# Optimization experiments

Hardware: AMD Instinct MI355X
Metric: run time of the kernel (lower is better)

## Reference

```python
import jax, jax.numpy as jnp
import numpy as np

EPS = 0.001  # epsilon used by both custom layer norms in the source
B, T, D, H, O = 64, 1024, 128, 256, 64


def setup_inputs() -> dict:
    key = jax.random.key(0)
    ks = jax.random.split(key, 8)
    s = 0.05
    return {
        "x": jax.random.normal(ks[0], (B, T, D), jnp.float32),
        "Wi": jax.random.normal(ks[1], (4 * H, D), jnp.float32) * s,   # input_weights
        "bi": jax.random.normal(ks[2], (4 * H,), jnp.float32) * s,
        "Wh": jax.random.normal(ks[3], (4 * H, H), jnp.float32) * s,   # hidden_weights
        "bh": jax.random.normal(ks[4], (4 * H,), jnp.float32) * s,
        "lna_gamma": jnp.ones((4 * H,), jnp.float32),
        "lna_beta": jnp.zeros((4 * H,), jnp.float32),
        "ln_gamma": jnp.ones((H,), jnp.float32),
        "ln_beta": jnp.zeros((H,), jnp.float32),
        "Wf": jax.random.normal(ks[5], (O, H), jnp.float32) * s,       # fc
        "bf": jax.random.normal(ks[6], (O,), jnp.float32) * s,
    }


def _ln(x, gamma, beta):
    # custom layer norm: mean/var over last axis, eps=1e-3 (no Bessel correction)
    m = jnp.mean(x, axis=-1, keepdims=True)
    xs = x - m
    v = jnp.mean(xs * xs, axis=-1, keepdims=True)
    return gamma * (xs / jnp.sqrt(v + EPS)) + beta


def reference(x, Wi, bi, Wh, bh, lna_gamma, lna_beta, ln_gamma, ln_beta, Wf, bf):
    b, t, d = x.shape
    h = Wh.shape[1]
    # precompute input projections for all timesteps: (T, B, 4H)
    xproj = jnp.einsum('btd,gd->tbg', x, Wi) + bi

    def step(carry, xp_t):
        hx, cx = carry                              # (B, H) each
        gates = xp_t + hx @ Wh.T + bh               # (B, 4H)
        # layer_norm_all: normalize each of the 4 gate blocks over H
        g4 = gates.reshape(b, 4, h)
        m = jnp.mean(g4, axis=-1, keepdims=True)
        gs = g4 - m
        v = jnp.mean(gs * gs, axis=-1, keepdims=True)
        gates = (gs / jnp.sqrt(v + EPS)).reshape(b, 4 * h) * lna_gamma + lna_beta
        ig, fg, cg, og = jnp.split(gates, 4, axis=1)
        ig = jax.nn.sigmoid(ig)
        fg = jax.nn.sigmoid(fg)
        cg = jnp.tanh(cg)
        og = jax.nn.sigmoid(og)
        cy = fg * cx + ig * cg
        hy = og * jnp.tanh(_ln(cy, ln_gamma, ln_beta))
        return (hy, cy), hy

    h0 = jnp.zeros((b, h), x.dtype)
    c0 = jnp.zeros((b, h), x.dtype)
    _, hs = jax.lax.scan(step, (h0, c0), xproj)     # hs: (T, B, H)
    out = hs.transpose(1, 0, 2)                     # (B, T, H)
    yhat = jax.nn.relu(out @ Wf.T + bf)             # (B, T, O)
    return yhat
```

## Files before the change

### kernel.cpp

```cpp
#include <hip/hip_runtime.h>

#define T_TOT 1024
#define BB 64
#define DD 128
#define HH 256
#define GG 1024
#define OO 64
#define LN_EPS 1e-3f
#define NV 24
#define NL 8

typedef unsigned int u32;
typedef _Float16 h2 __attribute__((ext_vector_type(2)));

__device__ __forceinline__ float fdot2(u32 a, u32 b, float c) {
  return __builtin_amdgcn_fdot2(__builtin_bit_cast(h2, a), __builtin_bit_cast(h2, b), c, false);
}
__device__ __forceinline__ u32 pkf16(float lo, float hi) {
  h2 v = { (_Float16)lo, (_Float16)hi };
  return __builtin_bit_cast(u32, v);
}
__device__ __forceinline__ float fast_sigmoid(float x) { return 1.0f / (1.0f + __expf(-x)); }
__device__ __forceinline__ float fast_tanh(float x) { return 2.0f / (1.0f + __expf(-2.0f * x)) - 1.0f; }

__global__ void prep_wh(const float* __restrict__ Wh, uint4* __restrict__ whp4) {
  int id = blockIdx.x * 256 + threadIdx.x;
  int kb = id >> 10, g = id & 1023;
  const float* p = Wh + (size_t)g * HH + kb * 8;
  uint4 o;
  o.x = pkf16(p[0], p[1]); o.y = pkf16(p[2], p[3]);
  o.z = pkf16(p[4], p[5]); o.w = pkf16(p[6], p[7]);
  whp4[id] = o;
}

__global__ void prep_wi(const float* __restrict__ Wi, uint4* __restrict__ wip4) {
  int id = blockIdx.x * 256 + threadIdx.x;
  int kp4 = id >> 10, g = id & 1023;
  const float* p = Wi + (size_t)g * DD + kp4 * 8;
  uint4 o;
  o.x = pkf16(p[0], p[1]); o.y = pkf16(p[2], p[3]);
  o.z = pkf16(p[4], p[5]); o.w = pkf16(p[6], p[7]);
  wip4[id] = o;
}

__global__ __launch_bounds__(256) void xproj_gemm(
    const float* __restrict__ x, const uint4* __restrict__ wip4,
    const float* __restrict__ bi, const float* __restrict__ bh,
    _Float16* __restrict__ xph, int m0) {
  __shared__ _Float16 xl[16][128];
  const int tid = threadIdx.x;
  const int mt = blockIdx.x, gt = blockIdx.y;
  const int g = gt * 256 + tid;
#pragma unroll
  for (int i = 0; i < 8; ++i) {
    int idx = i * 256 + tid;
    int p = idx >> 7, d = idx & 127;
    int m = m0 + mt * 16 + p;
    xl[p][d] = (_Float16)x[(size_t)(m & 63) * (T_TOT * DD) + (size_t)(m >> 6) * DD + d];
  }
  __syncthreads();
  float acc[16];
#pragma unroll
  for (int p = 0; p < 16; ++p) acc[p] = 0.f;
#pragma unroll
  for (int kp4 = 0; kp4 < 16; ++kp4) {
    uint4 w = wip4[kp4 * GG + g];
#pragma unroll
    for (int p = 0; p < 16; ++p) {
      uint4 hv = *(const uint4*)(&xl[p][kp4 * 8]);
      acc[p] = fdot2(w.x, hv.x, acc[p]);
      acc[p] = fdot2(w.y, hv.y, acc[p]);
      acc[p] = fdot2(w.z, hv.z, acc[p]);
      acc[p] = fdot2(w.w, hv.w, acc[p]);
    }
  }
  float bsum = bi[g] + bh[g];
#pragma unroll
  for (int p = 0; p < 16; ++p) {
    int ml = mt * 16 + p;
    xph[(size_t)ml * GG + g] = (_Float16)(acc[p] + bsum);
  }
}

__global__ __attribute__((amdgpu_flat_work_group_size(512, 512), amdgpu_waves_per_eu(2, 2)))
void lstm_scan(
    const uint4* __restrict__ whp4, const _Float16* __restrict__ xphf,
    const float* __restrict__ lna_g, const float* __restrict__ lna_b,
    const float* __restrict__ ln_g, const float* __restrict__ ln_b,
    _Float16* __restrict__ hs16,
    _Float16* __restrict__ hxst, float* __restrict__ cxst,
    int t0, int ct) {
  __shared__ uint4 wl[2 * NL * 512];
  __shared__ _Float16 hx16[HH];
  __shared__ float red[16];
  __shared__ float red2[8];
  __shared__ float gact[GG];

  const int tid = threadIdx.x;
  const int b = blockIdx.x;
  const int lane = tid & 63, wid = tid >> 6;
  const int q = wid >> 1, r = wid & 1;
  const int gA = q * 256 + r * 128 + lane;
  const int gB = gA + 64;

  uint4 wrA[NV], wrB[NV];
#pragma unroll
  for (int kb = 0; kb < NV; ++kb) {
    wrA[kb] = whp4[kb * 1024 + gA];
    wrB[kb] = whp4[kb * 1024 + gB];
  }
#pragma unroll
  for (int j = 0; j < NL; ++j) {
    wl[j * 512 + tid]        = whp4[(NV + j) * 1024 + gA];
    wl[(NL + j) * 512 + tid] = whp4[(NV + j) * 1024 + gB];
  }
  float lgA = lna_g[gA], lbA = lna_b[gA];
  float lgB = lna_g[gB], lbB = lna_b[gB];
  float lng = 0.f, lnb = 0.f, cx = 0.f;
  if (tid < HH) {
    lng = ln_g[tid]; lnb = ln_b[tid];
    if (t0 == 0) {
      hx16[tid] = (_Float16)0.f;
    } else {
      hx16[tid] = hxst[b * HH + tid]; cx = cxst[b * HH + tid];
    }
  }
  __syncthreads();

  const _Float16* xrA = xphf + b * GG + gA;
  const _Float16* xrB = xphf + b * GG + gB;
  _Float16* hsp = hs16 + (size_t)b * HH + (tid & 255);

  _Float16 xA16 = xrA[0], xB16 = xrB[0];
  for (int tl = 0; tl < ct; ++tl) {
    uint2 hp = *(const uint2*)(hx16 + 4 * lane);
    float accA = (float)xA16, accB = (float)xB16;
    if (tl + 1 < ct) {
      xA16 = xrA[(size_t)(tl + 1) * (BB * GG)];
      xB16 = xrB[(size_t)(tl + 1) * (BB * GG)];
    }
#pragma unroll
    for (int kb = 0; kb < NV; ++kb) {
      u32 h0 = (u32)__builtin_amdgcn_readlane((int)hp.x, 2 * kb);
      u32 h1 = (u32)__builtin_amdgcn_readlane((int)hp.y, 2 * kb);
      u32 h2 = (u32)__builtin_amdgcn_readlane((int)hp.x, 2 * kb + 1);
      u32 h3 = (u32)__builtin_amdgcn_readlane((int)hp.y, 2 * kb + 1);
      accA = fdot2(wrA[kb].x, h0, accA);
      accA = fdot2(wrA[kb].y, h1, accA);
      accA = fdot2(wrA[kb].z, h2, accA);
      accA = fdot2(wrA[kb].w, h3, accA);
      accB = fdot2(wrB[kb].x, h0, accB);
      accB = fdot2(wrB[kb].y, h1, accB);
      accB = fdot2(wrB[kb].z, h2, accB);
      accB = fdot2(wrB[kb].w, h3, accB);
    }
#pragma unroll
    for (int j = 0; j < NL; ++j) {
      const int kb = NV + j;
      u32 h0 = (u32)__builtin_amdgcn_readlane((int)hp.x, 2 * kb);
      u32 h1 = (u32)__builtin_amdgcn_readlane((int)hp.y, 2 * kb);
      u32 h2 = (u32)__builtin_amdgcn_readlane((int)hp.x, 2 * kb + 1);
      u32 h3 = (u32)__builtin_amdgcn_readlane((int)hp.y, 2 * kb + 1);
      uint4 wA = wl[j * 512 + tid];
      uint4 wB = wl[(NL + j) * 512 + tid];
      accA = fdot2(wA.x, h0, accA);
      accA = fdot2(wA.y, h1, accA);
      accA = fdot2(wA.z, h2, accA);
      accA = fdot2(wA.w, h3, accA);
      accB = fdot2(wB.x, h0, accB);
      accB = fdot2(wB.y, h1, accB);
      accB = fdot2(wB.z, h2, accB);
      accB = fdot2(wB.w, h3, accB);
    }

    float s = accA + accB, ss = accA * accA + accB * accB;
#pragma unroll
    for (int m = 1; m <= 32; m <<= 1) {
      s += __shfl_xor(s, m, 64);
      ss += __shfl_xor(ss, m, 64);
    }
    if (lane == 0) { red[wid] = s; red[8 + wid] = ss; }
    __syncthreads();
    float S  = red[2 * q] + red[2 * q + 1];
    float SS = red[8 + 2 * q] + red[8 + 2 * q + 1];
    float mean = S * (1.f / HH);
    float var = SS * (1.f / HH) - mean * mean;
    float rstd = rsqrtf(var + LN_EPS);
    float gnA = (accA - mean) * rstd * lgA + lbA;
    float gnB = (accB - mean) * rstd * lgB + lbB;
    float avA, avB;
    if (q == 2) { avA = fast_tanh(gnA); avB = fast_tanh(gnB); }
    else        { avA = fast_sigmoid(gnA); avB = fast_sigmoid(gnB); }
    gact[gA] = avA; gact[gB] = avB;
    __syncthreads();

    float cy = 0.f;
    if (tid < HH) {
      int h = tid;
      cy = gact[HH + h] * cx + gact[h] * gact[2 * HH + h];
      cx = cy;
      float s2 = cy, ss2 = cy * cy;
#pragma unroll
      for (int m = 1; m <= 32; m <<= 1) {
        s2 += __shfl_xor(s2, m, 64);
        ss2 += __shfl_xor(ss2, m, 64);
      }
      if (lane == 0) { red2[wid] = s2; red2[4 + wid] = ss2; }
    }
    __syncthreads();
    if (tid < HH) {
      int h = tid;
      float S2  = red2[0] + red2[1] + red2[2] + red2[3];
      float SS2 = red2[4] + red2[5] + red2[6] + red2[7];
      float mc = S2 * (1.f / HH);
      float vc = SS2 * (1.f / HH) - mc * mc;
      float cyn = (cy - mc) * rsqrtf(vc + LN_EPS) * lng + lnb;
      float hy = gact[3 * HH + h] * fast_tanh(cyn);
      hx16[h] = (_Float16)hy;
      hsp[(size_t)(t0 + tl) * (BB * HH)] = (_Float16)hy;
    }
    __syncthreads();
  }
  if (tid < HH) { hxst[b * HH + tid] = hx16[tid]; cxst[b * HH + tid] = cx; }
}

__global__ __launch_bounds__(256) void out_gemm(
    const _Float16* __restrict__ hs16, const float* __restrict__ Wf,
    const float* __restrict__ bf, float* __restrict__ out) {
  __shared__ u32 wfl[128][64];
  __shared__ u32 hsl[16][132];
  const int tid = threadIdx.x;
  const int mbase = blockIdx.x * 16;
#pragma unroll
  for (int i = 0; i < 32; ++i) {
    int idx = i * 256 + tid;
    int kp = idx >> 6, o = idx & 63;
    wfl[kp][o] = pkf16(Wf[o * HH + kp * 2], Wf[o * HH + kp * 2 + 1]);
  }
#pragma unroll
  for (int i = 0; i < 8; ++i) {
    int idx = i * 256 + tid;
    int p = idx >> 7, kp = idx & 127;
    hsl[p][kp] = *(const u32*)(hs16 + (size_t)(mbase + p) * HH + kp * 2);
  }
  __syncthreads();
  const int o = tid & 63, mi = tid >> 6;
  float bfo = bf[o];
#pragma unroll
  for (int mm = mi; mm < 16; mm += 4) {
    float a0 = bfo, a1 = 0.f, a2 = 0.f, a3 = 0.f;
#pragma unroll
    for (int kp = 0; kp < 128; kp += 4) {
      a0 = fdot2(wfl[kp + 0][o], hsl[mm][kp + 0], a0);
      a1 = fdot2(wfl[kp + 1][o], hsl[mm][kp + 1], a1);
      a2 = fdot2(wfl[kp + 2][o], hsl[mm][kp + 2], a2);
      a3 = fdot2(wfl[kp + 3][o], hsl[mm][kp + 3], a3);
    }
    float r = (a0 + a1) + (a2 + a3);
    int m = mbase + mm;
    out[(size_t)(m & 63) * (T_TOT * OO) + (size_t)(m >> 6) * OO + o] = fmaxf(r, 0.f);
  }
}

extern "C" void kernel_launch(void* const* d_in, const int* in_sizes, int n_in,
                              void* d_out, int out_size, void* d_ws, size_t ws_size,
                              hipStream_t stream) {
  if (n_in < 11) return;
  const float* x    = (const float*)d_in[0];
  const float* Wi   = (const float*)d_in[1];
  const float* bi   = (const float*)d_in[2];
  const float* Wh   = (const float*)d_in[3];
  const float* bh   = (const float*)d_in[4];
  const float* lnag = (const float*)d_in[5];
  const float* lnab = (const float*)d_in[6];
  const float* lng  = (const float*)d_in[7];
  const float* lnb  = (const float*)d_in[8];
  const float* Wf   = (const float*)d_in[9];
  const float* bf   = (const float*)d_in[10];
  float* out = (float*)d_out;

  char* ws = (char*)d_ws;
  uint4* whp4 = (uint4*)ws;
  uint4* wip4 = (uint4*)(ws + (512 << 10));
  _Float16* hs16 = (_Float16*)(ws + (1 << 20));
  _Float16* hxst = (_Float16*)(ws + (1 << 20) + (32 << 20));
  float* cxst = (float*)(ws + (1 << 20) + (32 << 20) + (64 << 10));
  const size_t xph_off = (size_t)35 << 20;
  _Float16* xph = (_Float16*)(ws + xph_off);

  size_t avail = ws_size > xph_off ? ws_size - xph_off : 0;
  int ct = T_TOT;
  while (ct > 1 && (size_t)ct * (BB * GG * 2) > avail) ct >>= 1;

  prep_wh<<<128, 256, 0, stream>>>(Wh, whp4);
  prep_wi<<<64, 256, 0, stream>>>(Wi, wip4);
  for (int t0 = 0; t0 < T_TOT; t0 += ct) {
    xproj_gemm<<<dim3((ct * BB) / 16, 4), 256, 0, stream>>>(x, wip4, bi, bh, xph, t0 * BB);
    lstm_scan<<<BB, 512, 0, stream>>>(whp4, xph, lnag, lnab, lng, lnb,
                                      hs16, hxst, cxst, t0, ct);
  }
  out_gemm<<<(T_TOT * BB) / 16, 256, 0, stream>>>(hs16, Wf, bf, out);
}
```

Measured before the change: 2.942 ms.

## Stream most recurrent weights from global/L2 each step instead of register residency

The recurrent weight slice per thread was held mostly in registers (24 chunks) with 8 chunks in LDS. Now only 3 chunks stay in registers, 9 go to LDS, and the remaining 20 chunks are reloaded from global memory (L2/cache) every timestep in three staged batches interleaved with the FMA work. The waves_per_eu constraint is replaced by plain launch bounds, which frees registers and may allow higher occupancy or avoid spills. The cost is a large per-step global/L2 load volume on the latency-critical serial recurrence, which may stall the dot products if the loads are not hidden.

```diff
diff --git a/kernel.cpp b/kernel.cpp
--- a/kernel.cpp
+++ b/kernel.cpp
@@ -7,8 +7,9 @@
 #define GG 1024
 #define OO 64
 #define LN_EPS 1e-3f
-#define NV 24
-#define NL 8
+#define NRG 3
+#define NLD 9
+#define KST 12
 
 typedef unsigned int u32;
 typedef _Float16 h2 __attribute__((ext_vector_type(2)));
@@ -22,6 +23,17 @@
 }
 __device__ __forceinline__ float fast_sigmoid(float x) { return 1.0f / (1.0f + __expf(-x)); }
 __device__ __forceinline__ float fast_tanh(float x) { return 2.0f / (1.0f + __expf(-2.0f * x)) - 1.0f; }
+
+#define DO_CHUNK(kb, wA, wB) do { \
+    u32 h0_ = (u32)__builtin_amdgcn_readlane((int)hp.x, 2 * (kb)); \
+    u32 h1_ = (u32)__builtin_amdgcn_readlane((int)hp.y, 2 * (kb)); \
+    u32 h2_ = (u32)__builtin_amdgcn_readlane((int)hp.x, 2 * (kb) + 1); \
+    u32 h3_ = (u32)__builtin_amdgcn_readlane((int)hp.y, 2 * (kb) + 1); \
+    accA = fdot2((wA).x, h0_, accA); accA = fdot2((wA).y, h1_, accA); \
+    accA = fdot2((wA).z, h2_, accA); accA = fdot2((wA).w, h3_, accA); \
+    accB = fdot2((wB).x, h0_, accB); accB = fdot2((wB).y, h1_, accB); \
+    accB = fdot2((wB).z, h2_, accB); accB = fdot2((wB).w, h3_, accB); \
+  } while (0)
 
 __global__ void prep_wh(const float* __restrict__ Wh, uint4* __restrict__ whp4) {
   int id = blockIdx.x * 256 + threadIdx.x;
@@ -82,15 +94,14 @@
   }
 }
 
-__global__ __attribute__((amdgpu_flat_work_group_size(512, 512), amdgpu_waves_per_eu(2, 2)))
-void lstm_scan(
+__global__ __launch_bounds__(512) void lstm_scan(
     const uint4* __restrict__ whp4, const _Float16* __restrict__ xphf,
     const float* __restrict__ lna_g, const float* __restrict__ lna_b,
     const float* __restrict__ ln_g, const float* __restrict__ ln_b,
     _Float16* __restrict__ hs16,
     _Float16* __restrict__ hxst, float* __restrict__ cxst,
     int t0, int ct) {
-  __shared__ uint4 wl[2 * NL * 512];
+  __shared__ uint4 wl[2 * NLD * 512];
   __shared__ _Float16 hx16[HH];
   __shared__ float red[16];
   __shared__ float red2[8];
@@ -103,36 +114,43 @@
   const int gA = q * 256 + r * 128 + lane;
   const int gB = gA + 64;
 
-  uint4 wrA[NV], wrB[NV];
-#pragma unroll
-  for (int kb = 0; kb < NV; ++kb) {
+  uint4 wrA[NRG], wrB[NRG];
+#pragma unroll
+  for (int kb = 0; kb < NRG; ++kb) {
     wrA[kb] = whp4[kb * 1024 + gA];
     wrB[kb] = whp4[kb * 1024 + gB];
   }
 #pragma unroll
-  for (int j = 0; j < NL; ++j) {
-    wl[j * 512 + tid]        = whp4[(NV + j) * 1024 + gA];
-    wl[(NL + j) * 512 + tid] = whp4[(NV + j) * 1024 + gB];
+  for (int j = 0; j < NLD; ++j) {
+    wl[j * 512 + tid]         = whp4[(NRG + j) * 1024 + gA];
+    wl[(NLD + j) * 512 + tid] = whp4[(NRG + j) * 1024 + gB];
   }
   float lgA = lna_g[gA], lbA = lna_b[gA];
   float lgB = lna_g[gB], lbB = lna_b[gB];
   float lng = 0.f, lnb = 0.f, cx = 0.f;
   if (tid < HH) {
     lng = ln_g[tid]; lnb = ln_b[tid];
-    if (t0 == 0) {
-      hx16[tid] = (_Float16)0.f;
-    } else {
-      hx16[tid] = hxst[b * HH + tid]; cx = cxst[b * HH + tid];
-    }
+    if (t0 == 0) hx16[tid] = (_Float16)0.f;
+    else { hx16[tid] = hxst[b * HH + tid]; cx = cxst[b * HH + tid]; }
   }
   __syncthreads();
 
   const _Float16* xrA = xphf + b * GG + gA;
   const _Float16* xrB = xphf + b * GG + gB;
   _Float16* hsp = hs16 + (size_t)b * HH + (tid & 255);
+  const uint4* stA0 = whp4 + KST * 1024 + gA;
+  const uint4* stB0 = stA0 + 64;
 
   _Float16 xA16 = xrA[0], xB16 = xrB[0];
   for (int tl = 0; tl < ct; ++tl) {
+    const uint4* sA = stA0;
+    const uint4* sB = stB0;
+    asm volatile("" : "+v"(sA), "+v"(sB));
+
+    uint4 g0A[6], g0B[6];
+#pragma unroll
+    for (int i = 0; i < 6; ++i) { g0A[i] = sA[i * 1024]; g0B[i] = sB[i * 1024]; }
+
     uint2 hp = *(const uint2*)(hx16 + 4 * lane);
     float accA = (float)xA16, accB = (float)xB16;
     if (tl + 1 < ct) {
@@ -140,38 +158,31 @@
       xB16 = xrB[(size_t)(tl + 1) * (BB * GG)];
     }
 #pragma unroll
-    for (int kb = 0; kb < NV; ++kb) {
-      u32 h0 = (u32)__builtin_amdgcn_readlane((int)hp.x, 2 * kb);
-      u32 h1 = (u32)__builtin_amdgcn_readlane((int)hp.y, 2 * kb);
-      u32 h2 = (u32)__builtin_amdgcn_readlane((int)hp.x, 2 * kb + 1);
-      u32 h3 = (u32)__builtin_amdgcn_readlane((int)hp.y, 2 * kb + 1);
-      accA = fdot2(wrA[kb].x, h0, accA);
-      accA = fdot2(wrA[kb].y, h1, accA);
-      accA = fdot2(wrA[kb].z, h2, accA);
-      accA = fdot2(wrA[kb].w, h3, accA);
-      accB = fdot2(wrB[kb].x, h0, accB);
-      accB = fdot2(wrB[kb].y, h1, accB);
-      accB = fdot2(wrB[kb].z, h2, accB);
-      accB = fdot2(wrB[kb].w, h3, accB);
-    }
-#pragma unroll
-    for (int j = 0; j < NL; ++j) {
-      const int kb = NV + j;
-      u32 h0 = (u32)__builtin_amdgcn_readlane((int)hp.x, 2 * kb);
-      u32 h1 = (u32)__builtin_amdgcn_readlane((int)hp.y, 2 * kb);
-      u32 h2 = (u32)__builtin_amdgcn_readlane((int)hp.x, 2 * kb + 1);
-      u32 h3 = (u32)__builtin_amdgcn_readlane((int)hp.y, 2 * kb + 1);
+    for (int kb = 0; kb < NRG; ++kb) DO_CHUNK(kb, wrA[kb], wrB[kb]);
+#pragma unroll
+    for (int j = 0; j < 5; ++j) {
       uint4 wA = wl[j * 512 + tid];
-      uint4 wB = wl[(NL + j) * 512 + tid];
-      accA = fdot2(wA.x, h0, accA);
-      accA = fdot2(wA.y, h1, accA);
-      accA = fdot2(wA.z, h2, accA);
-      accA = fdot2(wA.w, h3, accA);
-      accB = fdot2(wB.x, h0, accB);
-      accB = fdot2(wB.y, h1, accB);
-      accB = fdot2(wB.z, h2, accB);
-      accB = fdot2(wB.w, h3, accB);
-    }
+      uint4 wB = wl[(NLD + j) * 512 + tid];
+      DO_CHUNK(NRG + j, wA, wB);
+    }
+#pragma unroll
+    for (int i = 0; i < 6; ++i) DO_CHUNK(KST + i, g0A[i], g0B[i]);
+    uint4 g1A[7], g1B[7];
+#pragma unroll
+    for (int i = 0; i < 7; ++i) { g1A[i] = sA[(6 + i) * 1024]; g1B[i] = sB[(6 + i) * 1024]; }
+#pragma unroll
+    for (int j = 5; j < NLD; ++j) {
+      uint4 wA = wl[j * 512 + tid];
+      uint4 wB = wl[(NLD + j) * 512 + tid];
+      DO_CHUNK(NRG + j, wA, wB);
+    }
+#pragma unroll
+    for (int i = 0; i < 7; ++i) DO_CHUNK(KST + 6 + i, g1A[i], g1B[i]);
+    uint4 g2A[7], g2B[7];
+#pragma unroll
+    for (int i = 0; i < 7; ++i) { g2A[i] = sA[(13 + i) * 1024]; g2B[i] = sB[(13 + i) * 1024]; }
+#pragma unroll
+    for (int i = 0; i < 7; ++i) DO_CHUNK(KST + 13 + i, g2A[i], g2B[i]);
 
     float s = accA + accB, ss = accA * accA + accB * accB;
 #pragma unroll
```

Result: slower. 4.461 ms (+51.6%).
